# Kernel optimization log

Hardware: AMD Instinct MI355X
Metric: run time of the kernel (lower is better)

Reference implementation:

```python
import jax, jax.numpy as jnp
import numpy as np

NUM_NODES = 200000  # num_user + num_item
DIM_E = 64
NUM_EDGES = 600000
EPS = 1e-12
NEG_SLOPE = 0.01  # F.leaky_relu default


def setup_inputs() -> dict:
    key = jax.random.key(0)
    k1, k2, k3 = jax.random.split(key, 3)
    # xavier_normal on [N, D]: std = sqrt(2/(fan_in+fan_out))
    std = float(np.sqrt(2.0 / (NUM_NODES + DIM_E)))
    id_embedding = jax.random.normal(k1, (NUM_NODES, DIM_E), dtype=jnp.float32) * std
    edge_index = jax.random.randint(k2, (2, NUM_EDGES), 0, NUM_NODES, dtype=jnp.int64)
    weight_vector = jax.random.uniform(k3, (2 * NUM_EDGES, 1), dtype=jnp.float32)
    return {"id_embedding": id_embedding, "edge_index": edge_index,
            "weight_vector": weight_vector}


def _l2_normalize(x):
    # F.normalize(x, p=2, dim=1, eps=1e-12)
    n = jnp.sqrt(jnp.sum(x * x, axis=1, keepdims=True))
    return x / jnp.maximum(n, EPS)


def _leaky_relu(x):
    return jnp.where(x >= 0, x, NEG_SLOPE * x)


def reference(id_embedding, edge_index, weight_vector):
    N = id_embedding.shape[0]
    # symmetrize: cat(edge_index, edge_index[[1,0]])
    ei = jnp.concatenate([edge_index, edge_index[::-1]], axis=1)
    src, dst = ei[0], ei[1]  # messages flow src -> dst (PyG source_to_target)
    cnt = jax.ops.segment_sum(jnp.ones((src.shape[0],), jnp.float32), dst,
                              num_segments=N)[:, None]
    denom = jnp.maximum(cnt, 1.0)  # isolated nodes: sum is 0, mean defined as 0

    def conv(x):
        msg = x[src] * weight_vector            # gather + per-edge scale [2E, D]
        agg = jax.ops.segment_sum(msg, dst, num_segments=N)  # scatter-sum [N, D]
        return agg / denom                      # scatter-mean

    x = _l2_normalize(id_embedding)
    x1 = _leaky_relu(conv(x))
    x2 = _leaky_relu(conv(x1))
    return x + x1 + x2
```

## Files before the change

### kernel.cpp

```cpp
#include <hip/hip_runtime.h>
#include <hip/hip_fp16.h>

#define DIM 64
#define NEG_SLOPE 0.01f
#define BKT 256
#define TILE 2048

typedef unsigned u32;
typedef unsigned long long u64;


__global__ void k_norm_hist(const float* __restrict__ emb,
                            __half* __restrict__ x0h,
                            const int* __restrict__ p,
                            u32* __restrict__ mat,
                            int N, int E, int rb, int B, int nblkE) {
    if ((int)blockIdx.x < rb) {
        int lane = threadIdx.x & 63;
        int row  = blockIdx.x * 16 + (threadIdx.x >> 6) * 4 + (lane >> 4);
        int l16  = lane & 15;
        if (row >= N) return;
        float4 v = *(const float4*)(emb + (size_t)row * DIM + l16 * 4);
        float s = v.x * v.x + v.y * v.y + v.z * v.z + v.w * v.w;
        #pragma unroll
        for (int m = 1; m < 16; m <<= 1) s += __shfl_xor(s, m, 64);
        float inv = 1.0f / fmaxf(sqrtf(s), 1e-12f);
        union { uint2 u; __half2 h[2]; } pk;
        pk.h[0] = __floats2half2_rn(v.x * inv, v.y * inv);
        pk.h[1] = __floats2half2_rn(v.z * inv, v.w * inv);
        *(uint2*)(x0h + (size_t)row * DIM + l16 * 4) = pk.u;
    } else {
        __shared__ u32 hist[800];
        int blk = blockIdx.x - rb;
        int t = threadIdx.x;
        for (int i = t; i < B; i += 256) hist[i] = 0;
        __syncthreads();
        int base = blk * TILE;
        #pragma unroll
        for (int k = 0; k < TILE / 256; k++) {
            int e = base + k * 256 + t;
            if (e < 2 * E) {
                int dst = (e < E) ? p[e + E] : p[e - E];
                atomicAdd(&hist[(u32)dst >> 8], 1u);
            }
        }
        __syncthreads();
        for (int i = t; i < B; i += 256) mat[(size_t)i * nblkE + blk] = hist[i];
    }
}

__global__ void k_scan1(const u32* __restrict__ in, u32* __restrict__ out,
                        u32* __restrict__ bsum, int M) {
    __shared__ u32 sdata[256];
    int t = threadIdx.x;
    int base = blockIdx.x * TILE + t * 8;
    u32 v[8]; u32 tsum = 0;
    #pragma unroll
    for (int k = 0; k < 8; k++) {
        int i = base + k;
        v[k] = (i < M) ? in[i] : 0u;
        tsum += v[k];
    }
    sdata[t] = tsum;
    __syncthreads();
    for (int off = 1; off < 256; off <<= 1) {
        u32 x = (t >= off) ? sdata[t - off] : 0u;
        __syncthreads();
        sdata[t] += x;
        __syncthreads();
    }
    u32 run = sdata[t] - tsum;
    if (t == 255) bsum[blockIdx.x] = sdata[255];
    #pragma unroll
    for (int k = 0; k < 8; k++) {
        int i = base + k;
        if (i < M) out[i] = run;
        run += v[k];
    }
}

__global__ void k_scanfix(u32* __restrict__ mscan,
                          const u32* __restrict__ bsum, int nb, int M) {
    __shared__ u32 sdata[256];
    __shared__ u32 sexcl[256];
    int t = threadIdx.x;
    u32 v = (t < nb) ? bsum[t] : 0u;
    sdata[t] = v;
    __syncthreads();
    for (int off = 1; off < 256; off <<= 1) {
        u32 x = (t >= off) ? sdata[t - off] : 0u;
        __syncthreads();
        sdata[t] += x;
        __syncthreads();
    }
    sexcl[t] = sdata[t] - v;
    __syncthreads();
    int i = blockIdx.x * 256 + t;
    if (i < M) mscan[i] += sexcl[i >> 11];
}

__global__ void k_place(const int* __restrict__ p, const float* __restrict__ w,
                        const u32* __restrict__ mscan,
                        u32* __restrict__ pay, unsigned char* __restrict__ loc8,
                        int E, int nblkE, int B) {
    __shared__ u32 cur[800];
    int blk = blockIdx.x;
    int t = threadIdx.x;
    for (int i = t; i < B; i += 256) cur[i] = 0;
    __syncthreads();
    int base = blk * TILE;
    #pragma unroll
    for (int k = 0; k < TILE / 256; k++) {
        int e = base + k * 256 + t;
        if (e >= 2 * E) continue;
        int src = p[e];
        int dst = (e < E) ? p[e + E] : p[e - E];
        u32 bin = (u32)dst >> 8;
        u32 w14 = (u32)(w[e] * 16384.0f + 0.5f);
        if (w14 > 16383u) w14 = 16383u;
        u32 rank = atomicAdd(&cur[bin], 1u);
        u32 slot = mscan[(size_t)bin * nblkE + blk] + rank;
        pay[slot]  = ((u32)src << 14) | w14;
        loc8[slot] = (unsigned char)((u32)dst & (BKT - 1));
    }
}

__global__ void k_bucket(const u32* __restrict__ pay,
                         const unsigned char* __restrict__ loc8,
                         const u32* __restrict__ mscan,
                         u32* __restrict__ row_ptr,
                         u32* __restrict__ colw,
                         int N, int E, int B, int nblkE) {
    __shared__ u32 hist[BKT];
    __shared__ u32 excl[BKT];
    __shared__ u32 sdata[256];
    int b = blockIdx.x;
    int t = threadIdx.x;
    int node0 = b * BKT;
    int nnodes = N - node0; if (nnodes > BKT) nnodes = BKT;
    size_t flat0 = (size_t)b * nblkE;
    u32 seg_s = mscan[flat0];
    u32 seg_e = (b + 1 < B) ? mscan[flat0 + nblkE] : (u32)(2 * E);
    hist[t] = 0;
    __syncthreads();
    for (u32 j = seg_s + t; j < seg_e; j += 256)
        atomicAdd(&hist[loc8[j]], 1u);
    __syncthreads();
    u32 tsum = hist[t];
    sdata[t] = tsum;
    __syncthreads();
    for (int off = 1; off < 256; off <<= 1) {
        u32 x = (t >= off) ? sdata[t - off] : 0u;
        __syncthreads();
        sdata[t] += x;
        __syncthreads();
    }
    u32 texcl = sdata[t] - tsum;
    excl[t] = texcl;
    if (t < nnodes) row_ptr[node0 + t] = seg_s + texcl;
    if (b == 0 && t == 0) row_ptr[N] = (u32)(2 * E);
    __syncthreads();
    for (u32 j = seg_s + t; j < seg_e; j += 256) {
        u32 loc = loc8[j];
        u32 pos = atomicAdd(&excl[loc], 1u);
        colw[seg_s + pos] = pay[j];
    }
}


__device__ __forceinline__ void gather8(const __half* __restrict__ x,
                                        const u32* __restrict__ colw,
                                        u32 s, u32 e, int g, int sub,
                                        float acc[8]) {
    for (u32 base = s; base < e; base += 8) {
        int m = (int)(e - base); if (m > 8) m = 8;
        u32 u = 0;
        if (sub < m) u = colw[base + sub];
        int   cx = (int)(u >> 14);
        float cy = (float)(u & 16383u) * (1.0f / 16384.0f);
        for (int j = 0; j < m; j++) {
            int   sj = __shfl(cx, (g << 3) | j, 64);
            float wj = __shfl(cy, (g << 3) | j, 64);
            uint4 q = *(const uint4*)(x + (size_t)sj * DIM + sub * 8);
            const __half2* hp = (const __half2*)&q;
            #pragma unroll
            for (int k = 0; k < 4; k++) {
                float2 f = __half22float2(hp[k]);
                acc[2 * k]     += f.x * wj;
                acc[2 * k + 1] += f.y * wj;
            }
        }
    }
}

__global__ void k_conv1(const __half* __restrict__ x0h,
                        const u32* __restrict__ row_ptr,
                        const u32* __restrict__ colw,
                        __half* __restrict__ x1h, int N) {
    int wave = (blockIdx.x * 256 + threadIdx.x) >> 6;
    int g    = (threadIdx.x >> 3) & 7;
    int sub  = threadIdx.x & 7;
    int row  = wave * 8 + g;
    if (row >= N) return;
    u32 s = row_ptr[row], e = row_ptr[row + 1];
    float acc[8] = {0, 0, 0, 0, 0, 0, 0, 0};
    gather8(x0h, colw, s, e, g, sub, acc);
    float rdeno = 1.0f / fmaxf((float)(e - s), 1.0f);
    __half2 hv[4];
    #pragma unroll
    for (int k = 0; k < 4; k++) {
        float v0 = acc[2 * k] * rdeno;
        float v1 = acc[2 * k + 1] * rdeno;
        v0 = (v0 >= 0.0f) ? v0 : NEG_SLOPE * v0;
        v1 = (v1 >= 0.0f) ? v1 : NEG_SLOPE * v1;
        hv[k] = __floats2half2_rn(v0, v1);
    }
    *(uint4*)(x1h + (size_t)row * DIM + sub * 8) = *(const uint4*)hv;
}

__global__ void k_conv2(const __half* __restrict__ x0h,
                        const __half* __restrict__ x1h,
                        const u32* __restrict__ row_ptr,
                        const u32* __restrict__ colw,
                        float* __restrict__ out, int N) {
    int wave = (blockIdx.x * 256 + threadIdx.x) >> 6;
    int g    = (threadIdx.x >> 3) & 7;
    int sub  = threadIdx.x & 7;
    int row  = wave * 8 + g;
    if (row >= N) return;
    u32 s = row_ptr[row], e = row_ptr[row + 1];
    float acc[8] = {0, 0, 0, 0, 0, 0, 0, 0};
    gather8(x1h, colw, s, e, g, sub, acc);
    float rdeno = 1.0f / fmaxf((float)(e - s), 1.0f);
    uint4 q0 = *(const uint4*)(x0h + (size_t)row * DIM + sub * 8);
    uint4 q1 = *(const uint4*)(x1h + (size_t)row * DIM + sub * 8);
    const __half2* h0 = (const __half2*)&q0;
    const __half2* h1 = (const __half2*)&q1;
    float r[8];
    #pragma unroll
    for (int k = 0; k < 4; k++) {
        float2 a = __half22float2(h0[k]);
        float2 b = __half22float2(h1[k]);
        float x2a = acc[2 * k] * rdeno;
        float x2b = acc[2 * k + 1] * rdeno;
        x2a = (x2a >= 0.0f) ? x2a : NEG_SLOPE * x2a;
        x2b = (x2b >= 0.0f) ? x2b : NEG_SLOPE * x2b;
        r[2 * k]     = a.x + b.x + x2a;
        r[2 * k + 1] = a.y + b.y + x2b;
    }
    float* op = out + (size_t)row * DIM + sub * 8;
    *(float4*)(op)     = make_float4(r[0], r[1], r[2], r[3]);
    *(float4*)(op + 4) = make_float4(r[4], r[5], r[6], r[7]);
}

static inline size_t align16(size_t x) { return (x + 15) & ~(size_t)15; }

extern "C" void kernel_launch(void* const* d_in, const int* in_sizes, int n_in,
                              void* d_out, int out_size, void* d_ws, size_t ws_size,
                              hipStream_t stream) {
    const int N = in_sizes[0] / DIM;
    const int E = in_sizes[1] / 2;

    const float* emb = (const float*)d_in[0];
    const int*   ei  = (const int*)d_in[1];
    const float* w   = (const float*)d_in[2];
    float*       out = (float*)d_out;

    const int B     = (N + BKT - 1) / BKT;
    const int nblkE = (2 * E + TILE - 1) / TILE;
    const int M     = B * nblkE;
    const int nb1   = (M + TILE - 1) / TILE;
    const int rb    = (N + 15) / 16;
    const int cvb   = (N + 31) / 32;

    char* ws = (char*)d_ws;
    size_t off = 0;
    __half*        x0h    = (__half*)(ws + off);        off += align16((size_t)N * DIM * 2);
    __half*        x1h    = (__half*)(ws + off);        off += align16((size_t)N * DIM * 2);
    u32*           pay    = (u32*)(ws + off);           off += align16((size_t)2 * E * 4);
    unsigned char* loc8   = (unsigned char*)(ws + off); off += align16((size_t)2 * E);
    u32*           colw   = (u32*)(ws + off);           off += align16((size_t)2 * E * 4);
    u32*           mat    = (u32*)(ws + off);           off += align16((size_t)M * 4);
    u32*           mscan  = (u32*)(ws + off);           off += align16((size_t)M * 4);
    u32*           row_ptr= (u32*)(ws + off);           off += align16((size_t)(N + 1) * 4);
    u32*           bsum   = (u32*)(ws + off);           off += align16(256 * 4);

    k_norm_hist<<<rb + nblkE, 256, 0, stream>>>(emb, x0h, ei, mat, N, E, rb, B, nblkE);
    k_scan1  <<<nb1, 256, 0, stream>>>(mat, mscan, bsum, M);
    k_scanfix<<<(M + 255) / 256, 256, 0, stream>>>(mscan, bsum, nb1, M);
    k_place  <<<nblkE, 256, 0, stream>>>(ei, w, mscan, pay, loc8, E, nblkE, B);
    k_bucket <<<B, 256, 0, stream>>>(pay, loc8, mscan, row_ptr, colw, N, E, B, nblkE);

    k_conv1<<<cvb, 256, 0, stream>>>(x0h, row_ptr, colw, x1h, N);
    k_conv2<<<cvb, 256, 0, stream>>>(x0h, x1h, row_ptr, colw, out, N);
}
```

Measured before the change: 250.3 us.

## Process edge pairs together in histogram and placement with larger 512-thread tiles

The histogram and placement kernels now have each thread handle one original edge and emit both directed copies, reading src and dst once instead of twice. Blocks grow to 512 threads and each tile covers 4096 original edges, which shrinks nblkE and therefore the count matrix and the prefix-scan work. The normalization part handles 32 rows per block to match. The cost is more shared-memory atomics per thread and fewer blocks for the placement pass, which may reduce parallelism.

```diff
diff --git a/kernel.cpp b/kernel.cpp
--- a/kernel.cpp
+++ b/kernel.cpp
@@ -4,7 +4,8 @@
 #define DIM 64
 #define NEG_SLOPE 0.01f
 #define BKT 256
-#define TILE 2048
+#define TILEP 4096
+#define STILE 2048
 
 typedef unsigned u32;
 typedef unsigned long long u64;
@@ -15,9 +16,10 @@
                             const int* __restrict__ p,
                             u32* __restrict__ mat,
                             int N, int E, int rb, int B, int nblkE) {
+    int t = threadIdx.x;
     if ((int)blockIdx.x < rb) {
-        int lane = threadIdx.x & 63;
-        int row  = blockIdx.x * 16 + (threadIdx.x >> 6) * 4 + (lane >> 4);
+        int lane = t & 63;
+        int row  = blockIdx.x * 32 + (t >> 6) * 4 + (lane >> 4);
         int l16  = lane & 15;
         if (row >= N) return;
         float4 v = *(const float4*)(emb + (size_t)row * DIM + l16 * 4);
@@ -32,20 +34,21 @@
     } else {
         __shared__ u32 hist[800];
         int blk = blockIdx.x - rb;
-        int t = threadIdx.x;
-        for (int i = t; i < B; i += 256) hist[i] = 0;
-        __syncthreads();
-        int base = blk * TILE;
+        for (int i = t; i < B; i += 512) hist[i] = 0;
+        __syncthreads();
+        int base = blk * TILEP;
         #pragma unroll
-        for (int k = 0; k < TILE / 256; k++) {
-            int e = base + k * 256 + t;
-            if (e < 2 * E) {
-                int dst = (e < E) ? p[e + E] : p[e - E];
-                atomicAdd(&hist[(u32)dst >> 8], 1u);
+        for (int k = 0; k < TILEP / 512; k++) {
+            int pe = base + k * 512 + t;
+            if (pe < E) {
+                int a = p[pe];
+                int b = p[pe + E];
+                atomicAdd(&hist[(u32)b >> 8], 1u);
+                atomicAdd(&hist[(u32)a >> 8], 1u);
             }
         }
         __syncthreads();
-        for (int i = t; i < B; i += 256) mat[(size_t)i * nblkE + blk] = hist[i];
+        for (int i = t; i < B; i += 512) mat[(size_t)i * nblkE + blk] = hist[i];
     }
 }
 
@@ -53,7 +56,7 @@
                         u32* __restrict__ bsum, int M) {
     __shared__ u32 sdata[256];
     int t = threadIdx.x;
-    int base = blockIdx.x * TILE + t * 8;
+    int base = blockIdx.x * STILE + t * 8;
     u32 v[8]; u32 tsum = 0;
     #pragma unroll
     for (int k = 0; k < 8; k++) {
@@ -106,22 +109,29 @@
     __shared__ u32 cur[800];
     int blk = blockIdx.x;
     int t = threadIdx.x;
-    for (int i = t; i < B; i += 256) cur[i] = 0;
-    __syncthreads();
-    int base = blk * TILE;
-    #pragma unroll
-    for (int k = 0; k < TILE / 256; k++) {
-        int e = base + k * 256 + t;
-        if (e >= 2 * E) continue;
-        int src = p[e];
-        int dst = (e < E) ? p[e + E] : p[e - E];
-        u32 bin = (u32)dst >> 8;
-        u32 w14 = (u32)(w[e] * 16384.0f + 0.5f);
-        if (w14 > 16383u) w14 = 16383u;
+    for (int i = t; i < B; i += 512) cur[i] = 0;
+    __syncthreads();
+    int base = blk * TILEP;
+    #pragma unroll
+    for (int k = 0; k < TILEP / 512; k++) {
+        int pe = base + k * 512 + t;
+        if (pe >= E) continue;
+        int a = p[pe];
+        int b = p[pe + E];
+        float wf = w[pe];
+        float wb = w[pe + E];
+        u32 wf14 = (u32)(wf * 16384.0f + 0.5f); if (wf14 > 16383u) wf14 = 16383u;
+        u32 wb14 = (u32)(wb * 16384.0f + 0.5f); if (wb14 > 16383u) wb14 = 16383u;
+        u32 bin = (u32)b >> 8;
         u32 rank = atomicAdd(&cur[bin], 1u);
         u32 slot = mscan[(size_t)bin * nblkE + blk] + rank;
-        pay[slot]  = ((u32)src << 14) | w14;
-        loc8[slot] = (unsigned char)((u32)dst & (BKT - 1));
+        pay[slot]  = ((u32)a << 14) | wf14;
+        loc8[slot] = (unsigned char)((u32)b & (BKT - 1));
+        u32 bin2 = (u32)a >> 8;
+        u32 rank2 = atomicAdd(&cur[bin2], 1u);
+        u32 slot2 = mscan[(size_t)bin2 * nblkE + blk] + rank2;
+        pay[slot2]  = ((u32)b << 14) | wb14;
+        loc8[slot2] = (unsigned char)((u32)a & (BKT - 1));
     }
 }
 
@@ -267,10 +277,10 @@
     float*       out = (float*)d_out;
 
     const int B     = (N + BKT - 1) / BKT;
-    const int nblkE = (2 * E + TILE - 1) / TILE;
+    const int nblkE = (E + TILEP - 1) / TILEP;
     const int M     = B * nblkE;
-    const int nb1   = (M + TILE - 1) / TILE;
-    const int rb    = (N + 15) / 16;
+    const int nb1   = (M + STILE - 1) / STILE;
+    const int rb    = (N + 31) / 32;
     const int cvb   = (N + 31) / 32;
 
     char* ws = (char*)d_ws;
@@ -285,10 +295,10 @@
     u32*           row_ptr= (u32*)(ws + off);           off += align16((size_t)(N + 1) * 4);
     u32*           bsum   = (u32*)(ws + off);           off += align16(256 * 4);
 
-    k_norm_hist<<<rb + nblkE, 256, 0, stream>>>(emb, x0h, ei, mat, N, E, rb, B, nblkE);
+    k_norm_hist<<<rb + nblkE, 512, 0, stream>>>(emb, x0h, ei, mat, N, E, rb, B, nblkE);
     k_scan1  <<<nb1, 256, 0, stream>>>(mat, mscan, bsum, M);
     k_scanfix<<<(M + 255) / 256, 256, 0, stream>>>(mscan, bsum, nb1, M);
-    k_place  <<<nblkE, 256, 0, stream>>>(ei, w, mscan, pay, loc8, E, nblkE, B);
+    k_place  <<<nblkE, 512, 0, stream>>>(ei, w, mscan, pay, loc8, E, nblkE, B);
     k_bucket <<<B, 256, 0, stream>>>(pay, loc8, mscan, row_ptr, colw, N, E, B, nblkE);
 
     k_conv1<<<cvb, 256, 0, stream>>>(x0h, row_ptr, colw, x1h, N);
```

After: 244.2 us. 2.4% less time.
